# Kernel optimization log

Measured on AMD Instinct MI355X. Metric: run time of the kernel, lower is better.

Reference implementation:

```python
import jax, jax.numpy as jnp
import numpy as np

H = 512  # hidden_dimension
B = 32
S = 2048


def setup_inputs() -> dict:
    key = jax.random.key(0)
    k1, k2, k3, k4, k5, k6 = jax.random.split(key, 6)
    decoder_hide = jax.random.normal(k1, (B, H), dtype=jnp.float32)
    encoder_out = jax.random.normal(k2, (B, S, 2 * H), dtype=jnp.float32)
    mask = jax.random.randint(k3, (B, S), 0, 2, dtype=jnp.int32)
    bound = 1.0 / np.sqrt(3 * H)
    W_attn = jax.random.uniform(k4, (3 * H, H), minval=-bound, maxval=bound, dtype=jnp.float32)
    b_attn = jax.random.uniform(k5, (H,), minval=-bound, maxval=bound, dtype=jnp.float32)
    bound_v = 1.0 / np.sqrt(H)
    v_w = jax.random.uniform(k6, (H,), minval=-bound_v, maxval=bound_v, dtype=jnp.float32)
    return {"decoder_hide": decoder_hide, "encoder_out": encoder_out, "mask": mask,
            "W_attn": W_attn, "b_attn": b_attn, "v_w": v_w}


def reference(decoder_hide, encoder_out, mask, W_attn, b_attn, v_w):
    # Split the concat-linear: cat((h, enc)) @ W == h @ W[:H] + enc @ W[H:]
    W_h = W_attn[:H]        # [H, H]
    W_e = W_attn[H:]        # [2H, H]
    dec_proj = decoder_hide @ W_h + b_attn                 # [B, H]
    enc_proj = jnp.einsum('bse,eh->bsh', encoder_out, W_e)  # [B, S, H]
    energy = jnp.tanh(enc_proj + dec_proj[:, None, :])      # [B, S, H]
    attention = jnp.einsum('bsh,h->bs', energy, v_w)        # [B, S]
    attention = jnp.where(mask == 0, jnp.float32(-100000.0), attention)
    return jax.nn.softmax(attention, axis=1)
```

## Files before the change

### kernel.cpp

```cpp
#include <hip/hip_runtime.h>
#include <hip/hip_bf16.h>
#include <math.h>

#define Hdim 512
#define Bdim 32
#define Sdim 2048
#define Kdim 1024
#define Mtot (Bdim * Sdim)

#define BM 64
#define BN 512
#define BK 64

typedef __attribute__((ext_vector_type(8))) short short8;
typedef __attribute__((ext_vector_type(4))) float floatx4;

__device__ __forceinline__ short f2bf(float f) {
    union { float f; unsigned u; } v; v.f = f;
    unsigned r = v.u + 0x7fffu + ((v.u >> 16) & 1u);
    return (short)(r >> 16);
}

__device__ __forceinline__ short8 cvt8(float4 a, float4 b) {
    union { short8 s; __hip_bfloat162 h[4]; } u;
    u.h[0] = __float22bfloat162_rn(make_float2(a.x, a.y));
    u.h[1] = __float22bfloat162_rn(make_float2(a.z, a.w));
    u.h[2] = __float22bfloat162_rn(make_float2(b.x, b.y));
    u.h[3] = __float22bfloat162_rn(make_float2(b.z, b.w));
    return u.s;
}

__device__ __forceinline__ float fast_tanh(float x) {
    float ax = fabsf(x);
    float e  = __expf(-2.0f * ax);
    float r  = (1.0f - e) * __builtin_amdgcn_rcpf(1.0f + e);
    return copysignf(r, x);
}

__global__ __launch_bounds__(256) void prep_kernel(
    const float* __restrict__ W_attn, const float* __restrict__ dec,
    const float* __restrict__ b_attn, short* __restrict__ Wb,
    float* __restrict__ dec_proj)
{
    const int t = threadIdx.x;
    if (blockIdx.x < 512) {
        const float* We = W_attn + Hdim * Hdim;
        __shared__ short tile[32][33];
        const int k0 = (blockIdx.x >> 4) * 32;
        const int n0 = (blockIdx.x & 15) * 32;
        const int r = t >> 5, c = t & 31;
        #pragma unroll
        for (int rr = 0; rr < 4; ++rr)
            tile[r + rr * 8][c] = f2bf(We[(size_t)(k0 + r + rr * 8) * Hdim + n0 + c]);
        __syncthreads();
        #pragma unroll
        for (int rr = 0; rr < 4; ++rr)
            Wb[(size_t)(n0 + r + rr * 8) * Kdim + k0 + c] = tile[c][r + rr * 8];
    } else {
        __shared__ float partl[2][128];
        const int bid = blockIdx.x - 512;
        const int b  = bid >> 2;
        const int cb = bid & 3;
        const int c  = cb * 128 + (t & 127);
        const int kh = t >> 7;
        float acc = 0.0f;
        const int kbeg = kh * 256, kend = kbeg + 256;
        #pragma unroll 8
        for (int k = kbeg; k < kend; ++k)
            acc = fmaf(dec[b * Hdim + k], W_attn[(size_t)k * Hdim + c], acc);
        partl[kh][t & 127] = acc;
        __syncthreads();
        if (t < 128)
            dec_proj[b * Hdim + cb * 128 + t] = partl[0][t] + partl[1][t] + b_attn[cb * 128 + t];
    }
}

__global__ __launch_bounds__(256, 2) void scores_kernel(
    const float* __restrict__ enc,
    const short* __restrict__ Wb,
    const float* __restrict__ dec_proj,
    const float* __restrict__ v_w,
    float* __restrict__ scores)
{
    __shared__ __align__(16) short Asm[2 * BM * BK];
    __shared__ float redl[BM][4];

    const int t    = threadIdx.x;
    const int row0 = blockIdx.x * BM;
    const int b    = row0 / Sdim;

    const int w    = t >> 6;
    const int lane = t & 63;
    const int ln   = lane & 15;
    const int quad = lane >> 4;

    const int sm = t >> 2;
    const int sq = t & 3;
    const float* Ag = enc + (size_t)(row0 + sm) * Kdim + sq * 16;
    const int awr = sm * BK;
    const int aw0 = ((2 * sq)     ^ (sm & 7)) * 8;
    const int aw1 = ((2 * sq + 1) ^ (sm & 7)) * 8;

    int arow[4];
    #pragma unroll
    for (int i = 0; i < 4; ++i) arow[i] = (i * 16 + ln) * BK;
    const int pf0 = (quad       ^ (ln & 7)) * 8;
    const int pf1 = ((4 + quad) ^ (ln & 7)) * 8;

    const short* Bl = Wb + (size_t)(w * 128 + ln) * Kdim + quad * 8;

    floatx4 acc[4][8];
    #pragma unroll
    for (int i = 0; i < 4; ++i)
        #pragma unroll
        for (int j = 0; j < 8; ++j)
            acc[i][j] = (floatx4)(0.0f);

    float4 ra0, ra1, ra2, ra3;
    {
        const float4* g = (const float4*)Ag;
        ra0 = g[0]; ra1 = g[1]; ra2 = g[2]; ra3 = g[3];
    }

    for (int kt = 0; kt < Kdim; kt += BK) {
        short* Ab = Asm + ((kt >> 6) & 1) * (BM * BK);
        *(short8*)&Ab[awr + aw0] = cvt8(ra0, ra1);
        *(short8*)&Ab[awr + aw1] = cvt8(ra2, ra3);
        __syncthreads();

        if (kt + BK < Kdim) {
            const float4* g = (const float4*)(Ag + kt + BK);
            ra0 = g[0]; ra1 = g[1]; ra2 = g[2]; ra3 = g[3];
        }

        #pragma unroll
        for (int f = 0; f < 2; ++f) {
            const int pf = f ? pf1 : pf0;
            short8 af[4], bfr[8];
            #pragma unroll
            for (int j = 0; j < 8; ++j)
                bfr[j] = *(const short8*)(Bl + (size_t)j * 16 * Kdim + kt + f * 32);
            #pragma unroll
            for (int i = 0; i < 4; ++i) af[i] = *(const short8*)&Ab[arow[i] + pf];
            #pragma unroll
            for (int i = 0; i < 4; ++i)
                #pragma unroll
                for (int j = 0; j < 8; ++j)
                    acc[i][j] = __builtin_amdgcn_mfma_f32_16x16x32_bf16(
                                    af[i], bfr[j], acc[i][j], 0, 0, 0);
        }
    }

    float dpv[8], vwv[8];
    #pragma unroll
    for (int j = 0; j < 8; ++j) {
        int col = w * 128 + j * 16 + ln;
        dpv[j] = dec_proj[b * Hdim + col];
        vwv[j] = v_w[col];
    }
    #pragma unroll
    for (int i = 0; i < 4; ++i) {
        #pragma unroll
        for (int reg = 0; reg < 4; ++reg) {
            float s = 0.0f;
            #pragma unroll
            for (int j = 0; j < 8; ++j) {
                float x = acc[i][j][reg] + dpv[j];
                s = fmaf(vwv[j], fast_tanh(x), s);
            }
            s += __shfl_xor(s, 1, 64);
            s += __shfl_xor(s, 2, 64);
            s += __shfl_xor(s, 4, 64);
            s += __shfl_xor(s, 8, 64);
            if (ln == 0)
                redl[i * 16 + quad * 4 + reg][w] = s;
        }
    }
    __syncthreads();
    if (t < BM)
        scores[row0 + t] = redl[t][0] + redl[t][1] + redl[t][2] + redl[t][3];
}

__global__ __launch_bounds__(256) void softmax_kernel(
    const float* __restrict__ scores, const int* __restrict__ mask,
    float* __restrict__ out)
{
    __shared__ float sred[8];
    const int b = blockIdx.x;
    const int t = threadIdx.x;
    const int lane = t & 63;
    const int wid  = t >> 6;

    float x[8];
    float m = -1e30f;
    #pragma unroll
    for (int j = 0; j < 8; ++j) {
        int idx = b * Sdim + j * 256 + t;
        float v = scores[idx];
        if (mask[idx] == 0) v = -100000.0f;
        x[j] = v;
        m = fmaxf(m, v);
    }
    #pragma unroll
    for (int off = 32; off >= 1; off >>= 1)
        m = fmaxf(m, __shfl_xor(m, off, 64));
    if (lane == 0) sred[wid] = m;
    __syncthreads();
    m = fmaxf(fmaxf(sred[0], sred[1]), fmaxf(sred[2], sred[3]));

    float s = 0.0f;
    #pragma unroll
    for (int j = 0; j < 8; ++j) {
        float e = __expf(x[j] - m);
        x[j] = e;
        s += e;
    }
    #pragma unroll
    for (int off = 32; off >= 1; off >>= 1)
        s += __shfl_xor(s, off, 64);
    if (lane == 0) sred[4 + wid] = s;
    __syncthreads();
    s = sred[4] + sred[5] + sred[6] + sred[7];

    const float inv = 1.0f / s;
    #pragma unroll
    for (int j = 0; j < 8; ++j)
        out[b * Sdim + j * 256 + t] = x[j] * inv;
}

extern "C" void kernel_launch(void* const* d_in, const int* in_sizes, int n_in,
                              void* d_out, int out_size, void* d_ws, size_t ws_size,
                              hipStream_t stream) {
    const float* dec  = (const float*)d_in[0];
    const float* enc  = (const float*)d_in[1];
    const int*   mask = (const int*)  d_in[2];
    const float* W    = (const float*)d_in[3];
    const float* ba   = (const float*)d_in[4];
    const float* vw   = (const float*)d_in[5];
    float* out = (float*)d_out;

    float* dec_proj = (float*)d_ws;
    short* Wb       = (short*)(dec_proj + Bdim * Hdim);
    float* scores   = (float*)(Wb + Hdim * Kdim);

    prep_kernel<<<640, 256, 0, stream>>>(W, dec, ba, Wb, dec_proj);
    scores_kernel<<<Mtot / BM, 256, 0, stream>>>(enc, Wb, dec_proj, vw, scores);
    softmax_kernel<<<Bdim, 256, 0, stream>>>(scores, mask, out);
}
```

Baseline: 468.8 us.

## Split scores GEMM across 8 waves with 64-column tiles per wave

```diff
diff --git a/kernel.cpp b/kernel.cpp
--- a/kernel.cpp
+++ b/kernel.cpp
@@ -9,7 +9,6 @@
 #define Mtot (Bdim * Sdim)
 
 #define BM 64
-#define BN 512
 #define BK 64
 
 typedef __attribute__((ext_vector_type(8))) short short8;
@@ -75,7 +74,7 @@
     }
 }
 
-__global__ __launch_bounds__(256, 2) void scores_kernel(
+__global__ __launch_bounds__(512, 4) void scores_kernel(
     const float* __restrict__ enc,
     const short* __restrict__ Wb,
     const float* __restrict__ dec_proj,
@@ -83,7 +82,7 @@
     float* __restrict__ scores)
 {
     __shared__ __align__(16) short Asm[2 * BM * BK];
-    __shared__ float redl[BM][4];
+    __shared__ float redl[BM][8];
 
     const int t    = threadIdx.x;
     const int row0 = blockIdx.x * BM;
@@ -94,12 +93,10 @@
     const int ln   = lane & 15;
     const int quad = lane >> 4;
 
-    const int sm = t >> 2;
-    const int sq = t & 3;
-    const float* Ag = enc + (size_t)(row0 + sm) * Kdim + sq * 16;
-    const int awr = sm * BK;
-    const int aw0 = ((2 * sq)     ^ (sm & 7)) * 8;
-    const int aw1 = ((2 * sq + 1) ^ (sm & 7)) * 8;
+    const int sm = t >> 3;
+    const int sq = t & 7;
+    const float* Ag = enc + (size_t)(row0 + sm) * Kdim + sq * 8;
+    const int awo = sm * BK + ((sq ^ (sm & 7)) * 8);
 
     int arow[4];
     #pragma unroll
@@ -107,54 +104,62 @@
     const int pf0 = (quad       ^ (ln & 7)) * 8;
     const int pf1 = ((4 + quad) ^ (ln & 7)) * 8;
 
-    const short* Bl = Wb + (size_t)(w * 128 + ln) * Kdim + quad * 8;
-
-    floatx4 acc[4][8];
+    const short* Bl = Wb + (size_t)(w * 64 + ln) * Kdim + quad * 8;
+
+    floatx4 acc[4][4];
     #pragma unroll
     for (int i = 0; i < 4; ++i)
         #pragma unroll
-        for (int j = 0; j < 8; ++j)
+        for (int j = 0; j < 4; ++j)
             acc[i][j] = (floatx4)(0.0f);
 
-    float4 ra0, ra1, ra2, ra3;
+    float4 ra0, ra1;
     {
         const float4* g = (const float4*)Ag;
-        ra0 = g[0]; ra1 = g[1]; ra2 = g[2]; ra3 = g[3];
+        ra0 = g[0]; ra1 = g[1];
     }
 
     for (int kt = 0; kt < Kdim; kt += BK) {
         short* Ab = Asm + ((kt >> 6) & 1) * (BM * BK);
-        *(short8*)&Ab[awr + aw0] = cvt8(ra0, ra1);
-        *(short8*)&Ab[awr + aw1] = cvt8(ra2, ra3);
+        *(short8*)&Ab[awo] = cvt8(ra0, ra1);
         __syncthreads();
+
+        short8 b0[4], b1[4];
+        #pragma unroll
+        for (int j = 0; j < 4; ++j)
+            b0[j] = *(const short8*)(Bl + (size_t)j * 16 * Kdim + kt);
+        #pragma unroll
+        for (int j = 0; j < 4; ++j)
+            b1[j] = *(const short8*)(Bl + (size_t)j * 16 * Kdim + kt + 32);
 
         if (kt + BK < Kdim) {
             const float4* g = (const float4*)(Ag + kt + BK);
-            ra0 = g[0]; ra1 = g[1]; ra2 = g[2]; ra3 = g[3];
+            ra0 = g[0]; ra1 = g[1];
         }
 
-        #pragma unroll
-        for (int f = 0; f < 2; ++f) {
-            const int pf = f ? pf1 : pf0;
-            short8 af[4], bfr[8];
+        short8 af[4];
+        #pragma unroll
+        for (int i = 0; i < 4; ++i) af[i] = *(const short8*)&Ab[arow[i] + pf0];
+        #pragma unroll
+        for (int i = 0; i < 4; ++i)
             #pragma unroll
-            for (int j = 0; j < 8; ++j)
-                bfr[j] = *(const short8*)(Bl + (size_t)j * 16 * Kdim + kt + f * 32);
+            for (int j = 0; j < 4; ++j)
+                acc[i][j] = __builtin_amdgcn_mfma_f32_16x16x32_bf16(
+                                af[i], b0[j], acc[i][j], 0, 0, 0);
+        #pragma unroll
+        for (int i = 0; i < 4; ++i) af[i] = *(const short8*)&Ab[arow[i] + pf1];
+        #pragma unroll
+        for (int i = 0; i < 4; ++i)
             #pragma unroll
-            for (int i = 0; i < 4; ++i) af[i] = *(const short8*)&Ab[arow[i] + pf];
-            #pragma unroll
-            for (int i = 0; i < 4; ++i)
-                #pragma unroll
-                for (int j = 0; j < 8; ++j)
-                    acc[i][j] = __builtin_amdgcn_mfma_f32_16x16x32_bf16(
-                                    af[i], bfr[j], acc[i][j], 0, 0, 0);
-        }
-    }
-
-    float dpv[8], vwv[8];
-    #pragma unroll
-    for (int j = 0; j < 8; ++j) {
-        int col = w * 128 + j * 16 + ln;
+            for (int j = 0; j < 4; ++j)
+                acc[i][j] = __builtin_amdgcn_mfma_f32_16x16x32_bf16(
+                                af[i], b1[j], acc[i][j], 0, 0, 0);
+    }
+
+    float dpv[4], vwv[4];
+    #pragma unroll
+    for (int j = 0; j < 4; ++j) {
+        int col = w * 64 + j * 16 + ln;
         dpv[j] = dec_proj[b * Hdim + col];
         vwv[j] = v_w[col];
     }
@@ -164,7 +169,7 @@
         for (int reg = 0; reg < 4; ++reg) {
             float s = 0.0f;
             #pragma unroll
-            for (int j = 0; j < 8; ++j) {
+            for (int j = 0; j < 4; ++j) {
                 float x = acc[i][j][reg] + dpv[j];
                 s = fmaf(vwv[j], fast_tanh(x), s);
             }
@@ -177,8 +182,12 @@
         }
     }
     __syncthreads();
-    if (t < BM)
-        scores[row0 + t] = redl[t][0] + redl[t][1] + redl[t][2] + redl[t][3];
+    if (t < BM) {
+        float s = 0.0f;
+        #pragma unroll
+        for (int wv = 0; wv < 8; ++wv) s += redl[t][wv];
+        scores[row0 + t] = s;
+    }
 }
 
 __global__ __launch_bounds__(256) void softmax_kernel(
@@ -244,6 +253,6 @@
     float* scores   = (float*)(Wb + Hdim * Kdim);
 
     prep_kernel<<<640, 256, 0, stream>>>(W, dec, ba, Wb, dec_proj);
-    scores_kernel<<<Mtot / BM, 256, 0, stream>>>(enc, Wb, dec_proj, vw, scores);
+    scores_kernel<<<Mtot / BM, 512, 0, stream>>>(enc, Wb, dec_proj, vw, scores);
     softmax_kernel<<<Bdim, 256, 0, stream>>>(scores, mask, out);
 }
```

Measured after the change: 450.7 us. 3.8% less time.
